# Kernel optimization log

Hardware: AMD Instinct MI355X
Metric: run time of the kernel (lower is better)

The kernel has to match this reference:

```python
import jax, jax.numpy as jnp
import numpy as np

THR = 1.0   # snntorch Leaky default threshold
BETA = 0.9  # leak factor from the module


@jax.custom_vjp
def atan_spike(x):
    # Heaviside forward; ATan surrogate gradient (snntorch default alpha=2):
    # d/dx = 1 / (1 + (pi * x)^2)
    return (x > 0).astype(x.dtype)

def _atan_fwd(x):
    return (x > 0).astype(x.dtype), x

def _atan_bwd(x, g):
    return (g / (1.0 + (jnp.pi * x) ** 2),)

atan_spike.defvjp(_atan_fwd, _atan_bwd)


def setup_inputs() -> dict:
    key = jax.random.key(0)
    k0, k1, k2, k3, k4 = jax.random.split(key, 5)
    B, T, L = 256, 1000, 30  # 24 = L - 7 + 1 matches fc1 in_features 16*24
    out_c = 35
    x = jax.random.normal(k0, (B, T, L), dtype=jnp.float32)
    conv_w = jax.random.normal(k1, (16, 1, 7), dtype=jnp.float32) / np.float32(np.sqrt(7.0))
    conv_b = jax.random.normal(k2, (16,), dtype=jnp.float32) * 0.05
    fc_w = jax.random.normal(k3, (out_c, 16 * 24), dtype=jnp.float32) / np.float32(np.sqrt(384.0))
    fc_b = jax.random.normal(k4, (out_c,), dtype=jnp.float32) * 0.05
    return {"x": x, "conv_w": conv_w, "conv_b": conv_b, "fc_w": fc_w, "fc_b": fc_b}


def reference(x, conv_w, conv_b, fc_w, fc_b):
    B, T, L = x.shape
    # Conv1d has no recurrence -> hoist it out of the time loop, batched over B*T.
    cur1 = jax.lax.conv_general_dilated(
        x.reshape(B * T, 1, L), conv_w, window_strides=(1,), padding="VALID",
        dimension_numbers=("NCH", "OIH", "NCH"),
    ) + conv_b[None, :, None]                      # (B*T, 16, 24)
    Lo = cur1.shape[-1]
    cur1 = cur1.reshape(B, T, 16, Lo).transpose(1, 0, 2, 3)  # (T, B, 16, 24)
    out_c = fc_w.shape[0]

    def step(carry, c1):
        mem1, mem2 = carry
        # LIF1: reset-by-subtraction using detached spike of previous membrane
        r1 = jax.lax.stop_gradient((mem1 > THR).astype(mem1.dtype))
        mem1 = BETA * mem1 + c1 - r1 * THR
        spk1 = atan_spike(mem1 - THR)              # (B, 16, 24)
        c2 = spk1.reshape(B, 16 * Lo) @ fc_w.T + fc_b  # (B, out_c)
        # LIF2
        r2 = jax.lax.stop_gradient((mem2 > THR).astype(mem2.dtype))
        mem2 = BETA * mem2 + c2 - r2 * THR
        return (mem1, mem2), mem2

    init = (jnp.zeros((B, 16, Lo), x.dtype), jnp.zeros((B, out_c), x.dtype))
    _, mem2_rec = jax.lax.scan(step, init, cur1)   # (T, B, out_c)
    return mem2_rec.mean(axis=0)                   # (B, out_c)
```

## Files before the change

### kernel.cpp

```cpp
#include <hip/hip_runtime.h>

typedef _Float16 half8 __attribute__((ext_vector_type(8)));
typedef float f32x4 __attribute__((ext_vector_type(4)));

#define SPH  32
#define NPH  33
#define SPKW 392
#define XSW  32
#define C2W  48
#define TN   1000

__global__ __launch_bounds__(384) void snn_fwd(
    const float* __restrict__ x,
    const float* __restrict__ conv_w,
    const float* __restrict__ conv_b,
    const float* __restrict__ fc_w,
    const float* __restrict__ fc_b,
    float* __restrict__ out)
{
    __shared__ _Float16 spkL[SPH][SPKW];
    __shared__ float    xs[2][SPH][XSW];
    __shared__ float    c2L[SPH][C2W];

    const int tid  = threadIdx.x;
    const int b    = blockIdx.x;
    const int wid  = tid >> 6;
    const int lane = tid & 63;

    const int ct = tid;
    const int c  = ct / 12;
    const int u  = ct % 12;
    float wk[7];
    float cb = 0.f;
    if (wid < 3) {
#pragma unroll
        for (int k = 0; k < 7; ++k) wk[k] = conv_w[c * 7 + k];
        cb = conv_b[c];
    }

    const int m  = wid - 3;
    const int nL = lane & 15;
    const int q  = lane >> 4;
    half8 A[12];
    if (wid >= 3) {
        const int o = m * 16 + nL;
#pragma unroll
        for (int kt = 0; kt < 12; ++kt) {
            half8 a;
#pragma unroll
            for (int j = 0; j < 8; ++j) {
                int K = kt * 32 + q * 8 + j;
                a[j] = (o < 35) ? (_Float16)fc_w[o * 384 + K] : (_Float16)0.f;
            }
            A[kt] = a;
        }
    }
    const float fcb = (wid == 3 && lane < 35) ? fc_b[lane] : 0.f;

    float m10 = 0.f, m11 = 0.f, sp0 = 0.f, sp1 = 0.f;
    float mem2 = 0.f, accO = 0.f;

    const float* xb = x + (size_t)b * (TN * 30);

    if (wid < 3) {
#pragma unroll
        for (int r = 0; r < 5; ++r) {
            int f = ct + 192 * r;
            xs[0][f / 30][f % 30] = xb[f];
        }
    }
    __syncthreads();

#pragma unroll 1
    for (int ph = 0; ph < NPH; ++ph) {
        float xr[5];

        if (wid < 3) {
            if (ph < NPH - 2) {
                const float* src = xb + (ph + 1) * (SPH * 30);
#pragma unroll
                for (int r = 0; r < 5; ++r) {
                    int f = ct + 192 * r;
                    int t = (ph + 1) * SPH + f / 30;
                    xr[r] = (t < TN) ? src[f] : 0.f;
                }
            }
        } else if (ph > 0) {
            half8 B0[12], B1[12];
#pragma unroll
            for (int kt = 0; kt < 12; ++kt) {
                B0[kt] = *(const half8*)&spkL[nL][kt * 32 + q * 8];
                B1[kt] = *(const half8*)&spkL[16 + nL][kt * 32 + q * 8];
            }
            f32x4 acc0 = {0.f, 0.f, 0.f, 0.f};
            f32x4 acc1 = {0.f, 0.f, 0.f, 0.f};
#pragma unroll
            for (int kt = 0; kt < 12; ++kt) {
                acc0 = __builtin_amdgcn_mfma_f32_16x16x32_f16(A[kt], B0[kt], acc0, 0, 0, 0);
                acc1 = __builtin_amdgcn_mfma_f32_16x16x32_f16(A[kt], B1[kt], acc1, 0, 0, 0);
            }
            *(f32x4*)&c2L[nL][m * 16 + q * 4]      = acc0;
            *(f32x4*)&c2L[16 + nL][m * 16 + q * 4] = acc1;
        }
        __syncthreads();

        if (wid < 3) {
            if (ph < NPH - 1) {
                const float* xrow = &xs[ph & 1][0][2 * u];
#pragma unroll 4
                for (int s = 0; s < SPH; ++s) {
                    const float2* x2 = (const float2*)(xrow + s * XSW);
                    float2 a0 = x2[0], a1 = x2[1], a2 = x2[2], a3 = x2[3];
                    float c1a = cb, c1b = cb;
                    c1a = fmaf(wk[0], a0.x, c1a);  c1b = fmaf(wk[0], a0.y, c1b);
                    c1a = fmaf(wk[1], a0.y, c1a);  c1b = fmaf(wk[1], a1.x, c1b);
                    c1a = fmaf(wk[2], a1.x, c1a);  c1b = fmaf(wk[2], a1.y, c1b);
                    c1a = fmaf(wk[3], a1.y, c1a);  c1b = fmaf(wk[3], a2.x, c1b);
                    c1a = fmaf(wk[4], a2.x, c1a);  c1b = fmaf(wk[4], a2.y, c1b);
                    c1a = fmaf(wk[5], a2.y, c1a);  c1b = fmaf(wk[5], a3.x, c1b);
                    c1a = fmaf(wk[6], a3.x, c1a);  c1b = fmaf(wk[6], a3.y, c1b);

                    m10 = fmaf(0.9f, m10, c1a - sp0);
                    m11 = fmaf(0.9f, m11, c1b - sp1);
                    sp0 = (m10 > 1.0f) ? 1.0f : 0.0f;
                    sp1 = (m11 > 1.0f) ? 1.0f : 0.0f;
                    unsigned pk = (m10 > 1.0f ? 0x3C00u : 0u) | (m11 > 1.0f ? 0x3C000000u : 0u);
                    *(unsigned*)&spkL[s][2 * ct] = pk;
                }
            }
            if (ph < NPH - 2) {
                float* dst = &xs[(ph + 1) & 1][0][0];
#pragma unroll
                for (int r = 0; r < 5; ++r) {
                    int f = ct + 192 * r;
                    dst[(f / 30) * XSW + (f % 30)] = xr[r];
                }
            }
        } else if (wid == 3 && lane < 35 && ph > 0) {
            const int tb = (ph - 1) * SPH;
#pragma unroll
            for (int s8 = 0; s8 < SPH; s8 += 8) {
                float v[8];
#pragma unroll
                for (int j = 0; j < 8; ++j) v[j] = c2L[s8 + j][lane] + fcb;
#pragma unroll
                for (int j = 0; j < 8; ++j) {
                    float r2 = (mem2 > 1.0f) ? 1.0f : 0.0f;
                    mem2 = 0.9f * mem2 + v[j] - r2;
                    if (tb + s8 + j < TN) accO += mem2;
                }
            }
        }
        __syncthreads();
    }

    if (wid == 3 && lane < 35) out[b * 35 + lane] = accO * (1.0f / (float)TN);
}

extern "C" void kernel_launch(void* const* d_in, const int* in_sizes, int n_in,
                              void* d_out, int out_size, void* d_ws, size_t ws_size,
                              hipStream_t stream) {
    const float* x      = (const float*)d_in[0];
    const float* conv_w = (const float*)d_in[1];
    const float* conv_b = (const float*)d_in[2];
    const float* fc_w   = (const float*)d_in[3];
    const float* fc_b   = (const float*)d_in[4];
    float* out          = (float*)d_out;

    snn_fwd<<<256, 384, 0, stream>>>(x, conv_w, conv_b, fc_w, fc_b, out);
}
```

Measured before the change: 178.1 us.

## Double-buffer spike and c2 tiles into a three-stage per-phase pipeline

Double-buffers the spike and fc-output shared-memory tiles so LIF1/conv, the MFMA fc layer and the LIF2 scan for different time chunks run in the same iteration. This removes the second barrier inside each phase, leaving one __syncthreads per iteration. In exchange it adds one extra pipeline iteration and uses more shared memory, which could lower occupancy. The LIF2 scan, which stays serial, now overlaps with the MFMA and conv waves instead of running after them.

```diff
diff --git a/kernel.cpp b/kernel.cpp
--- a/kernel.cpp
+++ b/kernel.cpp
@@ -4,7 +4,7 @@
 typedef float f32x4 __attribute__((ext_vector_type(4)));
 
 #define SPH  32
-#define NPH  33
+#define NIT  34
 #define SPKW 392
 #define XSW  32
 #define C2W  48
@@ -18,9 +18,9 @@
     const float* __restrict__ fc_b,
     float* __restrict__ out)
 {
-    __shared__ _Float16 spkL[SPH][SPKW];
+    __shared__ _Float16 spk[2][SPH][SPKW];
     __shared__ float    xs[2][SPH][XSW];
-    __shared__ float    c2L[SPH][C2W];
+    __shared__ float    c2L[2][SPH][C2W];
 
     const int tid  = threadIdx.x;
     const int b    = blockIdx.x;
@@ -72,11 +72,11 @@
     __syncthreads();
 
 #pragma unroll 1
-    for (int ph = 0; ph < NPH; ++ph) {
-        float xr[5];
-
+    for (int ph = 0; ph < NIT; ++ph) {
         if (wid < 3) {
-            if (ph < NPH - 2) {
+            float xr[5];
+            const bool stg = (ph <= 30);
+            if (stg) {
                 const float* src = xb + (ph + 1) * (SPH * 30);
 #pragma unroll
                 for (int r = 0; r < 5; ++r) {
@@ -85,28 +85,9 @@
                     xr[r] = (t < TN) ? src[f] : 0.f;
                 }
             }
-        } else if (ph > 0) {
-            half8 B0[12], B1[12];
-#pragma unroll
-            for (int kt = 0; kt < 12; ++kt) {
-                B0[kt] = *(const half8*)&spkL[nL][kt * 32 + q * 8];
-                B1[kt] = *(const half8*)&spkL[16 + nL][kt * 32 + q * 8];
-            }
-            f32x4 acc0 = {0.f, 0.f, 0.f, 0.f};
-            f32x4 acc1 = {0.f, 0.f, 0.f, 0.f};
-#pragma unroll
-            for (int kt = 0; kt < 12; ++kt) {
-                acc0 = __builtin_amdgcn_mfma_f32_16x16x32_f16(A[kt], B0[kt], acc0, 0, 0, 0);
-                acc1 = __builtin_amdgcn_mfma_f32_16x16x32_f16(A[kt], B1[kt], acc1, 0, 0, 0);
-            }
-            *(f32x4*)&c2L[nL][m * 16 + q * 4]      = acc0;
-            *(f32x4*)&c2L[16 + nL][m * 16 + q * 4] = acc1;
-        }
-        __syncthreads();
-
-        if (wid < 3) {
-            if (ph < NPH - 1) {
+            if (ph < 32) {
                 const float* xrow = &xs[ph & 1][0][2 * u];
+                _Float16* sdst = &spk[ph & 1][0][2 * ct];
 #pragma unroll 4
                 for (int s = 0; s < SPH; ++s) {
                     const float2* x2 = (const float2*)(xrow + s * XSW);
@@ -125,10 +106,10 @@
                     sp0 = (m10 > 1.0f) ? 1.0f : 0.0f;
                     sp1 = (m11 > 1.0f) ? 1.0f : 0.0f;
                     unsigned pk = (m10 > 1.0f ? 0x3C00u : 0u) | (m11 > 1.0f ? 0x3C000000u : 0u);
-                    *(unsigned*)&spkL[s][2 * ct] = pk;
+                    *(unsigned*)(sdst + s * SPKW) = pk;
                 }
             }
-            if (ph < NPH - 2) {
+            if (stg) {
                 float* dst = &xs[(ph + 1) & 1][0][0];
 #pragma unroll
                 for (int r = 0; r < 5; ++r) {
@@ -136,18 +117,40 @@
                     dst[(f / 30) * XSW + (f % 30)] = xr[r];
                 }
             }
-        } else if (wid == 3 && lane < 35 && ph > 0) {
-            const int tb = (ph - 1) * SPH;
+        } else {
+            if (ph >= 1 && ph <= 32) {
+                const _Float16* sb = &spk[(ph - 1) & 1][0][0];
+                half8 B0[12], B1[12];
 #pragma unroll
-            for (int s8 = 0; s8 < SPH; s8 += 8) {
-                float v[8];
+                for (int kt = 0; kt < 12; ++kt) {
+                    B0[kt] = *(const half8*)(sb + nL * SPKW + kt * 32 + q * 8);
+                    B1[kt] = *(const half8*)(sb + (16 + nL) * SPKW + kt * 32 + q * 8);
+                }
+                f32x4 acc0 = {0.f, 0.f, 0.f, 0.f};
+                f32x4 acc1 = {0.f, 0.f, 0.f, 0.f};
 #pragma unroll
-                for (int j = 0; j < 8; ++j) v[j] = c2L[s8 + j][lane] + fcb;
+                for (int kt = 0; kt < 12; ++kt) {
+                    acc0 = __builtin_amdgcn_mfma_f32_16x16x32_f16(A[kt], B0[kt], acc0, 0, 0, 0);
+                    acc1 = __builtin_amdgcn_mfma_f32_16x16x32_f16(A[kt], B1[kt], acc1, 0, 0, 0);
+                }
+                float* cd = &c2L[(ph - 1) & 1][0][0];
+                *(f32x4*)(cd + nL * C2W + m * 16 + q * 4)        = acc0;
+                *(f32x4*)(cd + (16 + nL) * C2W + m * 16 + q * 4) = acc1;
+            }
+            if (wid == 3 && lane < 35 && ph >= 2) {
+                const float* cs = &c2L[(ph - 2) & 1][0][0];
+                const int tb = (ph - 2) * SPH;
 #pragma unroll
-                for (int j = 0; j < 8; ++j) {
-                    float r2 = (mem2 > 1.0f) ? 1.0f : 0.0f;
-                    mem2 = 0.9f * mem2 + v[j] - r2;
-                    if (tb + s8 + j < TN) accO += mem2;
+                for (int s8 = 0; s8 < SPH; s8 += 8) {
+                    float v[8];
+#pragma unroll
+                    for (int j = 0; j < 8; ++j) v[j] = cs[(s8 + j) * C2W + lane] + fcb;
+#pragma unroll
+                    for (int j = 0; j < 8; ++j) {
+                        float r2 = (mem2 > 1.0f) ? 1.0f : 0.0f;
+                        mem2 = 0.9f * mem2 + v[j] - r2;
+                        if (tb + s8 + j < TN) accO += mem2;
+                    }
                 }
             }
         }
```

Result: faster. 169.1 us (-5.0%).
